# Kernel tuning notes

Hardware: AMD Instinct MI355X
Metric: run time of the kernel (lower is better)

Reference implementation:

```python
import jax, jax.numpy as jnp
import numpy as np

EPS = 1e-6
NUM_HEADS = 16


def _layernorm(x, g, b):
    m = jnp.mean(x, axis=-1, keepdims=True)
    v = jnp.mean(jnp.square(x - m), axis=-1, keepdims=True)
    return (x - m) * jax.lax.rsqrt(v + EPS) * g + b


def setup_inputs() -> dict:
    key = jax.random.key(0)
    ks = jax.random.split(key, 16)
    B, Lq, Lkv, D = 2, 2048, 4096, 2048
    Hd = D // NUM_HEADS
    s = 0.02
    return {
        "hidden_states": jax.random.normal(ks[0], (B, Lq, D), jnp.float32),
        "cross_attention_states": jax.random.normal(ks[1], (B, Lkv, D), jnp.float32),
        "q_w": jax.random.normal(ks[2], (D, D), jnp.float32) * s,
        "q_b": jnp.zeros((D,), jnp.float32),
        "k_w": jax.random.normal(ks[3], (D, D), jnp.float32) * s,
        "k_b": jnp.zeros((D,), jnp.float32),
        "v_w": jax.random.normal(ks[4], (D, D), jnp.float32) * s,
        "v_b": jnp.zeros((D,), jnp.float32),
        "o_w": jax.random.normal(ks[5], (D, D), jnp.float32) * s,
        "o_b": jnp.zeros((D,), jnp.float32),
        "qn_g": jnp.ones((Hd,), jnp.float32),
        "qn_b": jnp.zeros((Hd,), jnp.float32),
        "kn_g": jnp.ones((Hd,), jnp.float32),
        "kn_b": jnp.zeros((Hd,), jnp.float32),
    }


def reference(hidden_states, cross_attention_states,
              q_w, q_b, k_w, k_b, v_w, v_b, o_w, o_b,
              qn_g, qn_b, kn_g, kn_b):
    B, Lq, D = hidden_states.shape
    H = NUM_HEADS
    Hd = D // H
    scale = Hd ** -0.5

    # torch Linear: y = x @ W^T + b
    q = hidden_states @ q_w.T + q_b                        # [B,Lq,D]
    k = cross_attention_states @ k_w.T + k_b               # [B,Lkv,D]
    v = cross_attention_states @ v_w.T + v_b               # [B,Lkv,D]

    q = q.reshape(B, Lq, H, Hd).transpose(0, 2, 1, 3)      # [B,H,Lq,Hd]
    k = k.reshape(B, -1, H, Hd).transpose(0, 2, 1, 3)      # [B,H,Lkv,Hd]
    v = v.reshape(B, -1, H, Hd).transpose(0, 2, 1, 3)      # [B,H,Lkv,Hd]

    # per-head QK LayerNorm before scores
    q = _layernorm(q, qn_g, qn_b)
    k = _layernorm(k, kn_g, kn_b)

    attn_weights = jnp.einsum('bhqd,bhkd->bhqk', q, k) * scale
    attn_weights = jax.nn.softmax(attn_weights.astype(jnp.float32), axis=-1).astype(q.dtype)
    # dropout p=0.0 (inference) -> identity

    attn_output = jnp.einsum('bhqk,bhkd->bhqd', attn_weights, v)
    attn_output = attn_output.transpose(0, 2, 1, 3).reshape(B, Lq, D)
    attn_output = attn_output @ o_w.T + o_b
    return attn_output, attn_weights
```

## Files before the change

kernel.cpp:

```cpp
#include <hip/hip_runtime.h>
#include <cstdint>
#include <cstddef>

using u16 = unsigned short;
using f32x4 = __attribute__((ext_vector_type(4))) float;
using bf8   = __attribute__((ext_vector_type(8))) short;
using u32x4 = __attribute__((ext_vector_type(4))) unsigned;

#define DEVFN __device__ __forceinline__

constexpr int BB  = 2;
constexpr int LQ  = 2048;
constexpr int LKV = 4096;
constexpr int DD  = 2048;
constexpr int NH  = 16;
constexpr int HDm = 128;
constexpr float ATTN_SCALE = 0.08838834764831845f;
constexpr float LN_EPS = 1e-6f;
constexpr float LOG2E  = 1.4426950408889634f;
constexpr float SHIFT2 = 17.312340490667562f;

DEVFN u16 f2bf(float f) {
  unsigned u = __builtin_bit_cast(unsigned, f);
  u += 0x7fffu + ((u >> 16) & 1u);
  return (u16)(u >> 16);
}
DEVFN float bf2f(u16 h) { return __builtin_bit_cast(float, (unsigned)h << 16); }
DEVFN f32x4 mfma16(bf8 a, bf8 b, f32x4 c) {
  return __builtin_amdgcn_mfma_f32_16x16x32_bf16(a, b, c, 0, 0, 0);
}
DEVFN void gl16(const void* g, void* l) {
  __builtin_amdgcn_global_load_lds(
      (const __attribute__((address_space(1))) void*)g,
      (__attribute__((address_space(3))) void*)l, 16, 0, 0);
}
DEVFN void barrier_hard() {
  __builtin_amdgcn_s_barrier();
  __builtin_amdgcn_sched_barrier(0);
}

__global__ __launch_bounds__(256) void k_cvt(const float4* __restrict__ in,
                                             ushort4* __restrict__ out, int n4) {
  int i = blockIdx.x * 256 + threadIdx.x;
  if (i >= n4) return;
  float4 v = in[i];
  ushort4 o;
  o.x = f2bf(v.x); o.y = f2bf(v.y); o.z = f2bf(v.z); o.w = f2bf(v.w);
  out[i] = o;
}

template <int MODE>
__global__ __launch_bounds__(256) void k_gemm_nt(const u16* __restrict__ X,
                                                 const u16* __restrict__ Wt,
                                                 const float* __restrict__ bias,
                                                 const float* __restrict__ lng,
                                                 const float* __restrict__ lnb,
                                                 void* __restrict__ Y,
                                                 int M, int N, int K) {
  __shared__ __align__(16) u16 Sh[2][128 * 64];
  __shared__ float Sm[2][128], Sq[2][128];
  u16* As = Sh[0];
  u16* Bs = Sh[1];
  const int tid = threadIdx.x;
  const int w = tid >> 6, l = tid & 63;
  const int m0 = blockIdx.x * 128, n0 = blockIdx.y * 128;
  const int wr = w >> 1, wc = w & 1;
  const int lr = l & 15, lk = (l >> 4) * 8;
  const int rsw = (l & 7) << 3;
  const int srow = l >> 3;
  const int scb = (l & 7) * 16;
  f32x4 acc[4][4] = {};

  for (int k0 = 0; k0 < K; k0 += 64) {
#pragma unroll
    for (int i = 0; i < 4; ++i) {
      int rbase = w * 32 + i * 8;
      int row = rbase + srow;
      int cb = scb ^ ((row & 7) << 4);
      gl16((const char*)&X[(size_t)(m0 + row) * K + k0] + cb, &As[rbase * 64]);
      gl16((const char*)&Wt[(size_t)(n0 + row) * K + k0] + cb, &Bs[rbase * 64]);
    }
    __syncthreads();
    bf8 af[4][2], bfr[4][2];
#pragma unroll
    for (int mi = 0; mi < 4; ++mi)
#pragma unroll
      for (int kk = 0; kk < 2; ++kk)
        af[mi][kk] = *(const bf8*)&As[(wr * 64 + mi * 16 + lr) * 64 + ((kk * 32 + lk) ^ rsw)];
#pragma unroll
    for (int ni = 0; ni < 4; ++ni)
#pragma unroll
      for (int kk = 0; kk < 2; ++kk)
        bfr[ni][kk] = *(const bf8*)&Bs[(wc * 64 + ni * 16 + lr) * 64 + ((kk * 32 + lk) ^ rsw)];
#pragma unroll
    for (int kk = 0; kk < 2; ++kk)
#pragma unroll
      for (int mi = 0; mi < 4; ++mi)
#pragma unroll
        for (int ni = 0; ni < 4; ++ni)
          acc[mi][ni] = mfma16(af[mi][kk], bfr[ni][kk], acc[mi][ni]);
    __syncthreads();
  }
  const int lrg = (l >> 4) * 4;

  float bv[4];
#pragma unroll
  for (int ni = 0; ni < 4; ++ni) bv[ni] = bias[n0 + wc * 64 + ni * 16 + lr];
#pragma unroll
  for (int mi = 0; mi < 4; ++mi)
#pragma unroll
    for (int ni = 0; ni < 4; ++ni)
#pragma unroll
      for (int r = 0; r < 4; ++r) acc[mi][ni][r] += bv[ni];

  if constexpr (MODE == 2 || MODE == 3) {
#pragma unroll
    for (int mi = 0; mi < 4; ++mi) {
#pragma unroll
      for (int r = 0; r < 4; ++r) {
        float ps = 0.f, pq = 0.f;
#pragma unroll
        for (int ni = 0; ni < 4; ++ni) {
          float v = acc[mi][ni][r];
          ps += v; pq += v * v;
        }
#pragma unroll
        for (int m = 1; m < 16; m <<= 1) {
          ps += __shfl_xor(ps, m);
          pq += __shfl_xor(pq, m);
        }
        if (lr == 0) {
          int rl = wr * 64 + mi * 16 + lrg + r;
          Sm[wc][rl] = ps; Sq[wc][rl] = pq;
        }
      }
    }
    __syncthreads();
    float gv[4], bbv[4];
#pragma unroll
    for (int ni = 0; ni < 4; ++ni) {
      int c = wc * 64 + ni * 16 + lr;
      gv[ni] = lng[c]; bbv[ni] = lnb[c];
    }
#pragma unroll
    for (int mi = 0; mi < 4; ++mi)
#pragma unroll
      for (int r = 0; r < 4; ++r) {
        int rl = wr * 64 + mi * 16 + lrg + r;
        float mean = (Sm[0][rl] + Sm[1][rl]) * (1.f / 128.f);
        float var  = (Sq[0][rl] + Sq[1][rl]) * (1.f / 128.f) - mean * mean;
        float rs = rsqrtf(var + LN_EPS);
#pragma unroll
        for (int ni = 0; ni < 4; ++ni) {
          float o = (acc[mi][ni][r] - mean) * rs * gv[ni] + bbv[ni];
          if (MODE == 3) o *= ATTN_SCALE;
          acc[mi][ni][r] = o;
        }
      }
  }

  if constexpr (MODE == 4) {
    u16* T = &Sh[0][0];
#pragma unroll
    for (int mi = 0; mi < 4; ++mi)
#pragma unroll
      for (int ni = 0; ni < 4; ++ni)
#pragma unroll
        for (int r = 0; r < 4; ++r) {
          int mrow = wr * 64 + mi * 16 + lrg + r;
          int ncol = wc * 64 + ni * 16 + lr;
          T[mrow * 128 + (ncol ^ ((mrow & 7) << 3))] = f2bf(acc[mi][ni][r]);
        }
    __syncthreads();
    int hd = tid >> 1, half = tid & 1;
    int bq = m0 >> 12;
    int kvb = (m0 & (LKV - 1)) + half * 64;
    int hh = n0 >> 7;
    u16* vout = (u16*)Y + ((size_t)(bq * NH + hh) * HDm + hd) * LKV + kvb;
#pragma unroll
    for (int j8 = 0; j8 < 8; ++j8) {
      u16 tmp[8] __attribute__((aligned(16)));
#pragma unroll
      for (int j = 0; j < 8; ++j) {
        int kv = half * 64 + j8 * 8 + j;
        tmp[j] = T[kv * 128 + (hd ^ ((kv & 7) << 3))];
      }
      *(int4*)&vout[j8 * 8] = *(const int4*)tmp;
    }
    return;
  }

#pragma unroll
  for (int ni = 0; ni < 4; ++ni) {
    int n = n0 + wc * 64 + ni * 16 + lr;
#pragma unroll
    for (int mi = 0; mi < 4; ++mi) {
      int mb = m0 + wr * 64 + mi * 16 + lrg;
#pragma unroll
      for (int r = 0; r < 4; ++r) {
        float v = acc[mi][ni][r];
        if constexpr (MODE == 1)
          __builtin_nontemporal_store(v, &((float*)Y)[(size_t)(mb + r) * N + n]);
        else
          ((u16*)Y)[(size_t)(mb + r) * N + n] = f2bf(v);
      }
    }
  }
}

__global__ __launch_bounds__(512, 4) void k_attn(const u16* __restrict__ Qp,
                                                 const u16* __restrict__ Kp,
                                                 const u16* __restrict__ Vt,
                                                 float* __restrict__ Wout,
                                                 u16* __restrict__ AO) {
  const int g = blockIdx.x;
  const int work = (g & 7) * 64 + (g >> 3);
  const int bh = work >> 4;
  const int b = bh >> 4, h = bh & 15;
  const int q0 = (work & 15) * 128;
  const int tid = threadIdx.x, w = tid >> 6, l = tid & 63;
  const int lr = l & 15, lk = (l >> 4) * 8;
  const int gq = l >> 4;
  const int rsw = (l & 7) << 3;
  __shared__ __align__(16) u16 Ks[2][64 * 128];
  __shared__ __align__(16) u16 Vs[2][128 * 64];

  bf8 qf[4];
  {
    const u16* qb = &Qp[((size_t)b * LQ + q0 + w * 16 + lr) * DD + h * HDm];
#pragma unroll
    for (int kc = 0; kc < 4; ++kc) qf[kc] = *(const bf8*)(qb + kc * 32 + lk);
  }
  const u16* Kb = Kp + (size_t)b * LKV * DD + h * HDm;
  const u16* Vb = Vt + (size_t)bh * HDm * LKV;

  auto stageK128 = [&](u16* buf, int kv0) {
#pragma unroll
    for (int i = 0; i < 4; ++i) {
      int rbase = i * 32 + w * 4;
      int row = rbase + (l >> 4);
      int cb = ((l & 15) * 16) ^ ((row & 7) << 4);
      gl16((const char*)(Kb + (size_t)(kv0 + row) * DD) + cb, &buf[rbase * 128]);
    }
  };
  auto stageK = [&](int buf, int kv0) {
#pragma unroll
    for (int i = 0; i < 2; ++i) {
      int rbase = i * 32 + w * 4;
      int row = rbase + (l >> 4);
      int cb = ((l & 15) * 16) ^ ((row & 7) << 4);
      gl16((const char*)(Kb + (size_t)(kv0 + row) * DD) + cb, &Ks[buf][rbase * 128]);
    }
  };
  auto stageV = [&](int buf, int kv0) {
#pragma unroll
    for (int i = 0; i < 2; ++i) {
      int rbase = i * 64 + w * 8;
      int row = rbase + (l >> 3);
      int cb = ((l & 7) * 16) ^ ((row & 7) << 4);
      gl16((const char*)(Vb + (size_t)row * LKV + kv0) + cb, &Vs[buf][rbase * 64]);
    }
  };

  u16* bufA0 = &Ks[0][0];
  u16* bufA1 = &Vs[0][0];
  float lsum = 0.f;
  stageK128(bufA0, 0);
  asm volatile("s_waitcnt vmcnt(0)" ::: "memory");
  barrier_hard();
  for (int t = 0; t < 32; ++t) {
    const u16* kb = (t & 1) ? bufA1 : bufA0;
    if (t < 31) stageK128((t & 1) ? bufA0 : bufA1, (t + 1) * 128);
    f32x4 s8[8];
    __builtin_amdgcn_s_setprio(1);
#pragma unroll
    for (int ni = 0; ni < 8; ++ni) {
      s8[ni] = f32x4{0.f, 0.f, 0.f, 0.f};
#pragma unroll
      for (int kc = 0; kc < 4; ++kc) {
        bf8 kf = *(const bf8*)&kb[(ni * 16 + lr) * 128 + ((kc * 32 + lk) ^ rsw)];
        s8[ni] = mfma16(kf, qf[kc], s8[ni]);
      }
    }
    __builtin_amdgcn_s_setprio(0);
#pragma unroll
    for (int ni = 0; ni < 8; ++ni)
#pragma unroll
      for (int r = 0; r < 4; ++r)
        lsum += exp2f(fmaf(s8[ni][r], LOG2E, -SHIFT2));
    asm volatile("s_waitcnt vmcnt(0)" ::: "memory");
    barrier_hard();
  }
  lsum += __shfl_xor(lsum, 16);
  lsum += __shfl_xor(lsum, 32);
  const float cr = -(SHIFT2 + __log2f(lsum));

  f32x4 oacc[8] = {};
  float* wq = Wout + ((size_t)bh * LQ + q0 + w * 16 + lr) * LKV;
  const int srcA = lr + ((gq & 1) << 5);
  const int srcB = srcA + 16;
  const bool hi = (gq >> 1) != 0;

  stageK(0, 0); stageV(0, 0);
  asm volatile("s_waitcnt vmcnt(0)" ::: "memory");
  barrier_hard();
  for (int t = 0; t < 64; ++t) {
    const int cur = t & 1;
    const int kv0 = t * 64;
    if (t < 63) { stageK(cur ^ 1, kv0 + 64); stageV(cur ^ 1, kv0 + 64); }
    f32x4 s[4];
    __builtin_amdgcn_s_setprio(1);
#pragma unroll
    for (int ni = 0; ni < 4; ++ni) {
      s[ni] = f32x4{0.f, 0.f, 0.f, 0.f};
#pragma unroll
      for (int kc = 0; kc < 4; ++kc) {
        bf8 kf = *(const bf8*)&Ks[cur][(ni * 16 + lr) * 128 + ((kc * 32 + lk) ^ rsw)];
        s[ni] = mfma16(kf, qf[kc], s[ni]);
      }
    }
    __builtin_amdgcn_s_setprio(0);
    unsigned pk2[4][2];
#pragma unroll
    for (int ni = 0; ni < 4; ++ni) {
      float p0 = exp2f(fmaf(s[ni][0], LOG2E, cr));
      float p1 = exp2f(fmaf(s[ni][1], LOG2E, cr));
      float p2 = exp2f(fmaf(s[ni][2], LOG2E, cr));
      float p3 = exp2f(fmaf(s[ni][3], LOG2E, cr));
      f32x4 pv4 = {p0, p1, p2, p3};
      __builtin_nontemporal_store(pv4, (f32x4*)(wq + kv0 + ni * 16 + 4 * gq));
      pk2[ni][0] = (unsigned)f2bf(p0) | ((unsigned)f2bf(p1) << 16);
      pk2[ni][1] = (unsigned)f2bf(p2) | ((unsigned)f2bf(p3) << 16);
    }
#pragma unroll
    for (int kk = 0; kk < 2; ++kk) {
      unsigned xa0 = __shfl(pk2[2 * kk][0], srcA), xa1 = __shfl(pk2[2 * kk][1], srcA);
      unsigned ya0 = __shfl(pk2[2 * kk + 1][0], srcA), ya1 = __shfl(pk2[2 * kk + 1][1], srcA);
      unsigned xb0 = __shfl(pk2[2 * kk][0], srcB), xb1 = __shfl(pk2[2 * kk][1], srcB);
      unsigned yb0 = __shfl(pk2[2 * kk + 1][0], srcB), yb1 = __shfl(pk2[2 * kk + 1][1], srcB);
      u32x4 pf32 = { hi ? ya0 : xa0, hi ? ya1 : xa1, hi ? yb0 : xb0, hi ? yb1 : xb1 };
      bf8 pf = __builtin_bit_cast(bf8, pf32);
      __builtin_amdgcn_s_setprio(1);
#pragma unroll
      for (int c = 0; c < 8; ++c) {
        bf8 vf = *(const bf8*)&Vs[cur][(c * 16 + lr) * 64 + ((kk * 32 + lk) ^ rsw)];
        oacc[c] = mfma16(pf, vf, oacc[c]);
      }
      __builtin_amdgcn_s_setprio(0);
    }
    asm volatile("s_waitcnt vmcnt(4)" ::: "memory");
    barrier_hard();
  }

#pragma unroll
  for (int c = 0; c < 8; ++c)
#pragma unroll
    for (int r = 0; r < 4; ++r)
      AO[((size_t)b * LQ + q0 + w * 16 + 4 * gq + r) * DD + h * HDm + c * 16 + lr] =
          f2bf(oacc[c][r]);
}

extern "C" void kernel_launch(void* const* d_in, const int* in_sizes, int n_in,
                              void* d_out, int out_size, void* d_ws, size_t ws_size,
                              hipStream_t stream) {
  const float* hs   = (const float*)d_in[0];
  const float* cas  = (const float*)d_in[1];
  const float* q_w  = (const float*)d_in[2];
  const float* q_b  = (const float*)d_in[3];
  const float* k_w  = (const float*)d_in[4];
  const float* k_b  = (const float*)d_in[5];
  const float* v_w  = (const float*)d_in[6];
  const float* v_b  = (const float*)d_in[7];
  const float* o_w  = (const float*)d_in[8];
  const float* o_b  = (const float*)d_in[9];
  const float* qn_g = (const float*)d_in[10];
  const float* qn_b = (const float*)d_in[11];
  const float* kn_g = (const float*)d_in[12];
  const float* kn_b = (const float*)d_in[13];

  float* out_attn = (float*)d_out;
  float* out_w    = out_attn + (size_t)BB * LQ * DD;

  constexpr size_t SZ_Q  = (size_t)BB * LQ * DD * 2;
  constexpr size_t SZ_KV = (size_t)BB * LKV * DD * 2;
  constexpr size_t SZ_W  = (size_t)DD * DD * 2;
  char* p = (char*)d_ws;
  u16* hsb  = (u16*)p;              p += SZ_Q;
  u16* casb = (u16*)p;              p += SZ_KV;
  u16* qwb  = (u16*)p;              p += SZ_W;
  u16* kwb  = (u16*)p;              p += SZ_W;
  u16* vwb  = (u16*)p;              p += SZ_W;
  u16* owb  = (u16*)p;              p += SZ_W;
  u16* Qp   = (u16*)p;              p += SZ_Q;
  u16* Kp   = (u16*)p;              p += SZ_KV;
  u16* Vtp  = (u16*)p;              p += SZ_KV;
  u16* AO   = (u16*)p;              p += SZ_Q;

  auto cvt = [&](const float* src, u16* dst, size_t n) {
    int n4 = (int)(n / 4);
    k_cvt<<<dim3((n4 + 255) / 256), dim3(256), 0, stream>>>(
        (const float4*)src, (ushort4*)dst, n4);
  };
  cvt(hs,  hsb,  (size_t)BB * LQ * DD);
  cvt(cas, casb, (size_t)BB * LKV * DD);
  cvt(q_w, qwb, (size_t)DD * DD);
  cvt(k_w, kwb, (size_t)DD * DD);
  cvt(v_w, vwb, (size_t)DD * DD);
  cvt(o_w, owb, (size_t)DD * DD);

  k_gemm_nt<3><<<dim3(BB * LQ / 128, DD / 128), dim3(256), 0, stream>>>(
      hsb, qwb, q_b, qn_g, qn_b, Qp, BB * LQ, DD, DD);
  k_gemm_nt<2><<<dim3(BB * LKV / 128, DD / 128), dim3(256), 0, stream>>>(
      casb, kwb, k_b, kn_g, kn_b, Kp, BB * LKV, DD, DD);
  k_gemm_nt<4><<<dim3(BB * LKV / 128, DD / 128), dim3(256), 0, stream>>>(
      casb, vwb, v_b, nullptr, nullptr, Vtp, BB * LKV, DD, DD);

  k_attn<<<dim3(LQ / 128 * BB * NH), dim3(512), 0, stream>>>(Qp, Kp, Vtp, out_w, AO);

  k_gemm_nt<1><<<dim3(BB * LQ / 128, DD / 128), dim3(256), 0, stream>>>(
      AO, owb, o_b, nullptr, nullptr, out_attn, BB * LQ, DD, DD);
}
```

Baseline: 753.5 us.

## Give each attention wave two 16-row Q tiles to reuse K/V fragments

The attention kernel drops from 8 to 4 waves per block. Each wave now handles 32 query rows as two 16-row sub-tiles, so every K and V fragment read from LDS feeds two MFMAs instead of one. Staging loops are rebalanced to load the same tiles with fewer threads, and the wait count is adjusted to match. This halves LDS read traffic per MFMA but doubles accumulator registers, and dropping the occupancy hint may lower occupancy and latency hiding.

After: 760.1 us. Within noise of the previous version (+0.9%).

```diff
diff --git a/kernel.cpp b/kernel.cpp
--- a/kernel.cpp
+++ b/kernel.cpp
@@ -208,11 +208,11 @@
   }
 }
 
-__global__ __launch_bounds__(512, 4) void k_attn(const u16* __restrict__ Qp,
-                                                 const u16* __restrict__ Kp,
-                                                 const u16* __restrict__ Vt,
-                                                 float* __restrict__ Wout,
-                                                 u16* __restrict__ AO) {
+__global__ __launch_bounds__(256) void k_attn(const u16* __restrict__ Qp,
+                                              const u16* __restrict__ Kp,
+                                              const u16* __restrict__ Vt,
+                                              float* __restrict__ Wout,
+                                              u16* __restrict__ AO) {
   const int g = blockIdx.x;
   const int work = (g & 7) * 64 + (g >> 3);
   const int bh = work >> 4;
@@ -225,78 +225,85 @@
   __shared__ __align__(16) u16 Ks[2][64 * 128];
   __shared__ __align__(16) u16 Vs[2][128 * 64];
 
-  bf8 qf[4];
-  {
-    const u16* qb = &Qp[((size_t)b * LQ + q0 + w * 16 + lr) * DD + h * HDm];
-#pragma unroll
-    for (int kc = 0; kc < 4; ++kc) qf[kc] = *(const bf8*)(qb + kc * 32 + lk);
+  bf8 qf[2][4];
+#pragma unroll
+  for (int qc = 0; qc < 2; ++qc) {
+    const u16* qb = &Qp[((size_t)b * LQ + q0 + w * 32 + qc * 16 + lr) * DD + h * HDm];
+#pragma unroll
+    for (int kc = 0; kc < 4; ++kc) qf[qc][kc] = *(const bf8*)(qb + kc * 32 + lk);
   }
   const u16* Kb = Kp + (size_t)b * LKV * DD + h * HDm;
   const u16* Vb = Vt + (size_t)bh * HDm * LKV;
 
+  auto stageK = [&](int buf, int kv0) {
+#pragma unroll
+    for (int i = 0; i < 4; ++i) {
+      int rbase = w * 16 + i * 4;
+      int row = rbase + (l >> 4);
+      int cb = ((l & 15) * 16) ^ ((row & 7) << 4);
+      gl16((const char*)(Kb + (size_t)(kv0 + row) * DD) + cb, &Ks[buf][rbase * 128]);
+    }
+  };
+  auto stageV = [&](int buf, int kv0) {
+#pragma unroll
+    for (int i = 0; i < 4; ++i) {
+      int rbase = w * 32 + i * 8;
+      int row = rbase + (l >> 3);
+      int cb = ((l & 7) * 16) ^ ((row & 7) << 4);
+      gl16((const char*)(Vb + (size_t)row * LKV + kv0) + cb, &Vs[buf][rbase * 64]);
+    }
+  };
   auto stageK128 = [&](u16* buf, int kv0) {
 #pragma unroll
-    for (int i = 0; i < 4; ++i) {
-      int rbase = i * 32 + w * 4;
+    for (int i = 0; i < 8; ++i) {
+      int rbase = w * 32 + i * 4;
       int row = rbase + (l >> 4);
       int cb = ((l & 15) * 16) ^ ((row & 7) << 4);
       gl16((const char*)(Kb + (size_t)(kv0 + row) * DD) + cb, &buf[rbase * 128]);
     }
   };
-  auto stageK = [&](int buf, int kv0) {
-#pragma unroll
-    for (int i = 0; i < 2; ++i) {
-      int rbase = i * 32 + w * 4;
-      int row = rbase + (l >> 4);
-      int cb = ((l & 15) * 16) ^ ((row & 7) << 4);
-      gl16((const char*)(Kb + (size_t)(kv0 + row) * DD) + cb, &Ks[buf][rbase * 128]);
-    }
-  };
-  auto stageV = [&](int buf, int kv0) {
-#pragma unroll
-    for (int i = 0; i < 2; ++i) {
-      int rbase = i * 64 + w * 8;
-      int row = rbase + (l >> 3);
-      int cb = ((l & 7) * 16) ^ ((row & 7) << 4);
-      gl16((const char*)(Vb + (size_t)row * LKV + kv0) + cb, &Vs[buf][rbase * 64]);
-    }
-  };
 
   u16* bufA0 = &Ks[0][0];
   u16* bufA1 = &Vs[0][0];
-  float lsum = 0.f;
+  float lsum[2] = {0.f, 0.f};
   stageK128(bufA0, 0);
   asm volatile("s_waitcnt vmcnt(0)" ::: "memory");
   barrier_hard();
   for (int t = 0; t < 32; ++t) {
     const u16* kb = (t & 1) ? bufA1 : bufA0;
     if (t < 31) stageK128((t & 1) ? bufA0 : bufA1, (t + 1) * 128);
-    f32x4 s8[8];
-    __builtin_amdgcn_s_setprio(1);
 #pragma unroll
     for (int ni = 0; ni < 8; ++ni) {
-      s8[ni] = f32x4{0.f, 0.f, 0.f, 0.f};
+      f32x4 s0 = {0.f, 0.f, 0.f, 0.f}, s1 = {0.f, 0.f, 0.f, 0.f};
+      __builtin_amdgcn_s_setprio(1);
 #pragma unroll
       for (int kc = 0; kc < 4; ++kc) {
         bf8 kf = *(const bf8*)&kb[(ni * 16 + lr) * 128 + ((kc * 32 + lk) ^ rsw)];
-        s8[ni] = mfma16(kf, qf[kc], s8[ni]);
-      }
-    }
-    __builtin_amdgcn_s_setprio(0);
-#pragma unroll
-    for (int ni = 0; ni < 8; ++ni)
-#pragma unroll
-      for (int r = 0; r < 4; ++r)
-        lsum += exp2f(fmaf(s8[ni][r], LOG2E, -SHIFT2));
+        s0 = mfma16(kf, qf[0][kc], s0);
+        s1 = mfma16(kf, qf[1][kc], s1);
+      }
+      __builtin_amdgcn_s_setprio(0);
+#pragma unroll
+      for (int r = 0; r < 4; ++r) {
+        lsum[0] += exp2f(fmaf(s0[r], LOG2E, -SHIFT2));
+        lsum[1] += exp2f(fmaf(s1[r], LOG2E, -SHIFT2));
+      }
+    }
     asm volatile("s_waitcnt vmcnt(0)" ::: "memory");
     barrier_hard();
   }
-  lsum += __shfl_xor(lsum, 16);
-  lsum += __shfl_xor(lsum, 32);
-  const float cr = -(SHIFT2 + __log2f(lsum));
-
-  f32x4 oacc[8] = {};
-  float* wq = Wout + ((size_t)bh * LQ + q0 + w * 16 + lr) * LKV;
+  float cr[2];
+#pragma unroll
+  for (int qc = 0; qc < 2; ++qc) {
+    float v = lsum[qc];
+    v += __shfl_xor(v, 16);
+    v += __shfl_xor(v, 32);
+    cr[qc] = -(SHIFT2 + __log2f(v));
+  }
+
+  f32x4 oacc[2][8] = {};
+  float* wq0 = Wout + ((size_t)bh * LQ + q0 + w * 32 + lr) * LKV;
+  float* wq1 = wq0 + (size_t)16 * LKV;
   const int srcA = lr + ((gq & 1) << 5);
   const int srcB = srcA + 16;
   const bool hi = (gq >> 1) != 0;
@@ -308,56 +315,69 @@
     const int cur = t & 1;
     const int kv0 = t * 64;
     if (t < 63) { stageK(cur ^ 1, kv0 + 64); stageV(cur ^ 1, kv0 + 64); }
-    f32x4 s[4];
+    f32x4 s[2][4];
     __builtin_amdgcn_s_setprio(1);
 #pragma unroll
     for (int ni = 0; ni < 4; ++ni) {
-      s[ni] = f32x4{0.f, 0.f, 0.f, 0.f};
+      s[0][ni] = f32x4{0.f, 0.f, 0.f, 0.f};
+      s[1][ni] = f32x4{0.f, 0.f, 0.f, 0.f};
 #pragma unroll
       for (int kc = 0; kc < 4; ++kc) {
         bf8 kf = *(const bf8*)&Ks[cur][(ni * 16 + lr) * 128 + ((kc * 32 + lk) ^ rsw)];
-        s[ni] = mfma16(kf, qf[kc], s[ni]);
+        s[0][ni] = mfma16(kf, qf[0][kc], s[0][ni]);
+        s[1][ni] = mfma16(kf, qf[1][kc], s[1][ni]);
       }
     }
     __builtin_amdgcn_s_setprio(0);
-    unsigned pk2[4][2];
-#pragma unroll
-    for (int ni = 0; ni < 4; ++ni) {
-      float p0 = exp2f(fmaf(s[ni][0], LOG2E, cr));
-      float p1 = exp2f(fmaf(s[ni][1], LOG2E, cr));
-      float p2 = exp2f(fmaf(s[ni][2], LOG2E, cr));
-      float p3 = exp2f(fmaf(s[ni][3], LOG2E, cr));
-      f32x4 pv4 = {p0, p1, p2, p3};
-      __builtin_nontemporal_store(pv4, (f32x4*)(wq + kv0 + ni * 16 + 4 * gq));
-      pk2[ni][0] = (unsigned)f2bf(p0) | ((unsigned)f2bf(p1) << 16);
-      pk2[ni][1] = (unsigned)f2bf(p2) | ((unsigned)f2bf(p3) << 16);
+    unsigned pk2[2][4][2];
+#pragma unroll
+    for (int qc = 0; qc < 2; ++qc) {
+      float* wq = qc ? wq1 : wq0;
+#pragma unroll
+      for (int ni = 0; ni < 4; ++ni) {
+        float p0 = exp2f(fmaf(s[qc][ni][0], LOG2E, cr[qc]));
+        float p1 = exp2f(fmaf(s[qc][ni][1], LOG2E, cr[qc]));
+        float p2 = exp2f(fmaf(s[qc][ni][2], LOG2E, cr[qc]));
+        float p3 = exp2f(fmaf(s[qc][ni][3], LOG2E, cr[qc]));
+        f32x4 pv4 = {p0, p1, p2, p3};
+        __builtin_nontemporal_store(pv4, (f32x4*)(wq + kv0 + ni * 16 + 4 * gq));
+        pk2[qc][ni][0] = (unsigned)f2bf(p0) | ((unsigned)f2bf(p1) << 16);
+        pk2[qc][ni][1] = (unsigned)f2bf(p2) | ((unsigned)f2bf(p3) << 16);
+      }
     }
 #pragma unroll
     for (int kk = 0; kk < 2; ++kk) {
-      unsigned xa0 = __shfl(pk2[2 * kk][0], srcA), xa1 = __shfl(pk2[2 * kk][1], srcA);
-      unsigned ya0 = __shfl(pk2[2 * kk + 1][0], srcA), ya1 = __shfl(pk2[2 * kk + 1][1], srcA);
-      unsigned xb0 = __shfl(pk2[2 * kk][0], srcB), xb1 = __shfl(pk2[2 * kk][1], srcB);
-      unsigned yb0 = __shfl(pk2[2 * kk + 1][0], srcB), yb1 = __shfl(pk2[2 * kk + 1][1], srcB);
-      u32x4 pf32 = { hi ? ya0 : xa0, hi ? ya1 : xa1, hi ? yb0 : xb0, hi ? yb1 : xb1 };
-      bf8 pf = __builtin_bit_cast(bf8, pf32);
+      bf8 pfq[2];
+#pragma unroll
+      for (int qc = 0; qc < 2; ++qc) {
+        unsigned xa0 = __shfl(pk2[qc][2 * kk][0], srcA), xa1 = __shfl(pk2[qc][2 * kk][1], srcA);
+        unsigned ya0 = __shfl(pk2[qc][2 * kk + 1][0], srcA), ya1 = __shfl(pk2[qc][2 * kk + 1][1], srcA);
+        unsigned xb0 = __shfl(pk2[qc][2 * kk][0], srcB), xb1 = __shfl(pk2[qc][2 * kk][1], srcB);
+        unsigned yb0 = __shfl(pk2[qc][2 * kk + 1][0], srcB), yb1 = __shfl(pk2[qc][2 * kk + 1][1], srcB);
+        u32x4 pf32 = { hi ? ya0 : xa0, hi ? ya1 : xa1, hi ? yb0 : xb0, hi ? yb1 : xb1 };
+        pfq[qc] = __builtin_bit_cast(bf8, pf32);
+      }
       __builtin_amdgcn_s_setprio(1);
 #pragma unroll
       for (int c = 0; c < 8; ++c) {
         bf8 vf = *(const bf8*)&Vs[cur][(c * 16 + lr) * 64 + ((kk * 32 + lk) ^ rsw)];
-        oacc[c] = mfma16(pf, vf, oacc[c]);
+        oacc[0][c] = mfma16(pfq[0], vf, oacc[0][c]);
+        oacc[1][c] = mfma16(pfq[1], vf, oacc[1][c]);
       }
       __builtin_amdgcn_s_setprio(0);
     }
-    asm volatile("s_waitcnt vmcnt(4)" ::: "memory");
+    asm volatile("s_waitcnt vmcnt(8)" ::: "memory");
     barrier_hard();
   }
 
 #pragma unroll
-  for (int c = 0; c < 8; ++c)
-#pragma unroll
-    for (int r = 0; r < 4; ++r)
-      AO[((size_t)b * LQ + q0 + w * 16 + 4 * gq + r) * DD + h * HDm + c * 16 + lr] =
-          f2bf(oacc[c][r]);
+  for (int qc = 0; qc < 2; ++qc)
+#pragma unroll
+    for (int c = 0; c < 8; ++c)
+#pragma unroll
+      for (int r = 0; r < 4; ++r)
+        AO[((size_t)b * LQ + q0 + w * 32 + qc * 16 + 4 * gq + r) * DD + h * HDm + c * 16 + lr] =
+            f2bf(oacc[qc][c][r]);
 }
 
 extern "C" void kernel_launch(void* const* d_in, const int* in_sizes, int n_in,
@@ -415,7 +435,7 @@
   k_gemm_nt<4><<<dim3(BB * LKV / 128, DD / 128), dim3(256), 0, stream>>>(
       casb, vwb, v_b, nullptr, nullptr, Vtp, BB * LKV, DD, DD);
 
-  k_attn<<<dim3(LQ / 128 * BB * NH), dim3(512), 0, stream>>>(Qp, Kp, Vtp, out_w, AO);
+  k_attn<<<dim3(LQ / 128 * BB * NH), dim3(256), 0, stream>>>(Qp, Kp, Vtp, out_w, AO);
 
   k_gemm_nt<1><<<dim3(BB * LQ / 128, DD / 128), dim3(256), 0, stream>>>(
       AO, owb, o_b, nullptr, nullptr, out_attn, BB * LQ, DD, DD);
```

## Split softmax row-sum pass into separate kernel with 256-row Q tiles; fuse conversions

Applied to the files above, without the earlier changes.

The first pass that computes softmax normalisers moves out of the attention kernel into its own kernel. That kernel processes 256 query rows per block and keeps two Q fragments per wave, so each staged K tile is reused twice. It writes per-row log constants to a workspace buffer, which the attention kernel then reads. The six fp32-to-bf16 conversion launches are merged into one segmented launch. This halves K reloads in the sum pass and removes launch overhead, at the cost of an extra kernel launch, a small global buffer, and a larger LDS footprint per block.

Result: slower. 796.2 us (+5.7%).

```diff
diff --git a/kernel.cpp b/kernel.cpp
--- a/kernel.cpp
+++ b/kernel.cpp
@@ -39,14 +39,22 @@
   __builtin_amdgcn_sched_barrier(0);
 }
 
-__global__ __launch_bounds__(256) void k_cvt(const float4* __restrict__ in,
-                                             ushort4* __restrict__ out, int n4) {
-  int i = blockIdx.x * 256 + threadIdx.x;
-  if (i >= n4) return;
-  float4 v = in[i];
+struct C6 {
+  const float4* s[6];
+  ushort4* d[6];
+  unsigned off[7];
+};
+__global__ __launch_bounds__(256) void k_cvt6(C6 a) {
+  unsigned gi = blockIdx.x * 256 + threadIdx.x;
+  if (gi >= a.off[6]) return;
+  int seg = 0;
+#pragma unroll
+  for (int i = 1; i < 6; ++i) seg += (gi >= a.off[i]);
+  unsigned j = gi - a.off[seg];
+  float4 v = a.s[seg][j];
   ushort4 o;
   o.x = f2bf(v.x); o.y = f2bf(v.y); o.z = f2bf(v.z); o.w = f2bf(v.w);
-  out[i] = o;
+  a.d[seg][j] = o;
 }
 
 template <int MODE>
@@ -208,9 +216,79 @@
   }
 }
 
+__global__ __launch_bounds__(512, 4) void k_sums(const u16* __restrict__ Qp,
+                                                 const u16* __restrict__ Kp,
+                                                 float* __restrict__ crg) {
+  const int g = blockIdx.x;
+  const int work = (g & 7) * 32 + (g >> 3);
+  const int bh = work >> 3;
+  const int b = bh >> 4, h = bh & 15;
+  const int q0 = (work & 7) * 256;
+  const int tid = threadIdx.x, w = tid >> 6, l = tid & 63;
+  const int lr = l & 15, lk = (l >> 4) * 8;
+  const int rsw = (l & 7) << 3;
+  __shared__ __align__(16) u16 Kt[2][128 * 128];
+
+  bf8 qf[2][4];
+#pragma unroll
+  for (int qc = 0; qc < 2; ++qc) {
+    const u16* qb = &Qp[((size_t)b * LQ + q0 + w * 32 + qc * 16 + lr) * DD + h * HDm];
+#pragma unroll
+    for (int kc = 0; kc < 4; ++kc) qf[qc][kc] = *(const bf8*)(qb + kc * 32 + lk);
+  }
+  const u16* Kb = Kp + (size_t)b * LKV * DD + h * HDm;
+
+  auto stage = [&](int buf, int kv0) {
+#pragma unroll
+    for (int i = 0; i < 4; ++i) {
+      int rbase = w * 16 + i * 4;
+      int row = rbase + (l >> 4);
+      int cb = ((l & 15) * 16) ^ ((row & 7) << 4);
+      gl16((const char*)(Kb + (size_t)(kv0 + row) * DD) + cb, &Kt[buf][rbase * 128]);
+    }
+  };
+
+  float lsum[2] = {0.f, 0.f};
+  stage(0, 0);
+  asm volatile("s_waitcnt vmcnt(0)" ::: "memory");
+  barrier_hard();
+  for (int t = 0; t < 32; ++t) {
+    const int cur = t & 1;
+    if (t < 31) stage(cur ^ 1, (t + 1) * 128);
+#pragma unroll
+    for (int ni = 0; ni < 8; ++ni) {
+      f32x4 s0 = {0.f, 0.f, 0.f, 0.f}, s1 = {0.f, 0.f, 0.f, 0.f};
+      __builtin_amdgcn_s_setprio(1);
+#pragma unroll
+      for (int kc = 0; kc < 4; ++kc) {
+        bf8 kf = *(const bf8*)&Kt[cur][(ni * 16 + lr) * 128 + ((kc * 32 + lk) ^ rsw)];
+        s0 = mfma16(kf, qf[0][kc], s0);
+        s1 = mfma16(kf, qf[1][kc], s1);
+      }
+      __builtin_amdgcn_s_setprio(0);
+#pragma unroll
+      for (int r = 0; r < 4; ++r) {
+        lsum[0] += exp2f(fmaf(s0[r], LOG2E, -SHIFT2));
+        lsum[1] += exp2f(fmaf(s1[r], LOG2E, -SHIFT2));
+      }
+    }
+    asm volatile("s_waitcnt vmcnt(0)" ::: "memory");
+    barrier_hard();
+  }
+#pragma unroll
+  for (int qc = 0; qc < 2; ++qc) {
+    float v = lsum[qc];
+    v += __shfl_xor(v, 16);
+    v += __shfl_xor(v, 32);
+    if (l < 16)
+      crg[(size_t)bh * LQ + q0 + w * 32 + qc * 16 + l] = -(SHIFT2 + __log2f(v));
+  }
+}
+
 __global__ __launch_bounds__(512, 4) void k_attn(const u16* __restrict__ Qp,
                                                  const u16* __restrict__ Kp,
                                                  const u16* __restrict__ Vt,
+                                                 const float* __restrict__ crg,
                                                  float* __restrict__ Wout,
                                                  u16* __restrict__ AO) {
   const int g = blockIdx.x;
@@ -231,18 +309,10 @@
 #pragma unroll
     for (int kc = 0; kc < 4; ++kc) qf[kc] = *(const bf8*)(qb + kc * 32 + lk);
   }
+  const float crv = crg[(size_t)bh * LQ + q0 + w * 16 + lr];
   const u16* Kb = Kp + (size_t)b * LKV * DD + h * HDm;
   const u16* Vb = Vt + (size_t)bh * HDm * LKV;
 
-  auto stageK128 = [&](u16* buf, int kv0) {
-#pragma unroll
-    for (int i = 0; i < 4; ++i) {
-      int rbase = i * 32 + w * 4;
-      int row = rbase + (l >> 4);
-      int cb = ((l & 15) * 16) ^ ((row & 7) << 4);
-      gl16((const char*)(Kb + (size_t)(kv0 + row) * DD) + cb, &buf[rbase * 128]);
-    }
-  };
   auto stageK = [&](int buf, int kv0) {
 #pragma unroll
     for (int i = 0; i < 2; ++i) {
@@ -261,39 +331,6 @@
       gl16((const char*)(Vb + (size_t)row * LKV + kv0) + cb, &Vs[buf][rbase * 64]);
     }
   };
-
-  u16* bufA0 = &Ks[0][0];
-  u16* bufA1 = &Vs[0][0];
-  float lsum = 0.f;
-  stageK128(bufA0, 0);
-  asm volatile("s_waitcnt vmcnt(0)" ::: "memory");
-  barrier_hard();
-  for (int t = 0; t < 32; ++t) {
-    const u16* kb = (t & 1) ? bufA1 : bufA0;
-    if (t < 31) stageK128((t & 1) ? bufA0 : bufA1, (t + 1) * 128);
-    f32x4 s8[8];
-    __builtin_amdgcn_s_setprio(1);
-#pragma unroll
-    for (int ni = 0; ni < 8; ++ni) {
-      s8[ni] = f32x4{0.f, 0.f, 0.f, 0.f};
-#pragma unroll
-      for (int kc = 0; kc < 4; ++kc) {
-        bf8 kf = *(const bf8*)&kb[(ni * 16 + lr) * 128 + ((kc * 32 + lk) ^ rsw)];
-        s8[ni] = mfma16(kf, qf[kc], s8[ni]);
-      }
-    }
-    __builtin_amdgcn_s_setprio(0);
-#pragma unroll
-    for (int ni = 0; ni < 8; ++ni)
-#pragma unroll
-      for (int r = 0; r < 4; ++r)
-        lsum += exp2f(fmaf(s8[ni][r], LOG2E, -SHIFT2));
-    asm volatile("s_waitcnt vmcnt(0)" ::: "memory");
-    barrier_hard();
-  }
-  lsum += __shfl_xor(lsum, 16);
-  lsum += __shfl_xor(lsum, 32);
-  const float cr = -(SHIFT2 + __log2f(lsum));
 
   f32x4 oacc[8] = {};
   float* wq = Wout + ((size_t)bh * LQ + q0 + w * 16 + lr) * LKV;
@@ -323,10 +360,10 @@
     unsigned pk2[4][2];
 #pragma unroll
     for (int ni = 0; ni < 4; ++ni) {
-      float p0 = exp2f(fmaf(s[ni][0], LOG2E, cr));
-      float p1 = exp2f(fmaf(s[ni][1], LOG2E, cr));
-      float p2 = exp2f(fmaf(s[ni][2], LOG2E, cr));
-      float p3 = exp2f(fmaf(s[ni][3], LOG2E, cr));
+      float p0 = exp2f(fmaf(s[ni][0], LOG2E, crv));
+      float p1 = exp2f(fmaf(s[ni][1], LOG2E, crv));
+      float p2 = exp2f(fmaf(s[ni][2], LOG2E, crv));
+      float p3 = exp2f(fmaf(s[ni][3], LOG2E, crv));
       f32x4 pv4 = {p0, p1, p2, p3};
       __builtin_nontemporal_store(pv4, (f32x4*)(wq + kv0 + ni * 16 + 4 * gq));
       pk2[ni][0] = (unsigned)f2bf(p0) | ((unsigned)f2bf(p1) << 16);
@@ -395,18 +432,26 @@
   u16* Kp   = (u16*)p;              p += SZ_KV;
   u16* Vtp  = (u16*)p;              p += SZ_KV;
   u16* AO   = (u16*)p;              p += SZ_Q;
-
-  auto cvt = [&](const float* src, u16* dst, size_t n) {
-    int n4 = (int)(n / 4);
-    k_cvt<<<dim3((n4 + 255) / 256), dim3(256), 0, stream>>>(
-        (const float4*)src, (ushort4*)dst, n4);
-  };
-  cvt(hs,  hsb,  (size_t)BB * LQ * DD);
-  cvt(cas, casb, (size_t)BB * LKV * DD);
-  cvt(q_w, qwb, (size_t)DD * DD);
-  cvt(k_w, kwb, (size_t)DD * DD);
-  cvt(v_w, vwb, (size_t)DD * DD);
-  cvt(o_w, owb, (size_t)DD * DD);
+  float* crg = (float*)p;           p += (size_t)BB * NH * LQ * 4;
+
+  constexpr unsigned HS4 = BB * LQ * DD / 4;
+  constexpr unsigned CAS4 = BB * LKV * DD / 4;
+  constexpr unsigned W4 = DD * DD / 4;
+  C6 a;
+  a.s[0] = (const float4*)hs;  a.d[0] = (ushort4*)hsb;
+  a.s[1] = (const float4*)cas; a.d[1] = (ushort4*)casb;
+  a.s[2] = (const float4*)q_w; a.d[2] = (ushort4*)qwb;
+  a.s[3] = (const float4*)k_w; a.d[3] = (ushort4*)kwb;
+  a.s[4] = (const float4*)v_w; a.d[4] = (ushort4*)vwb;
+  a.s[5] = (const float4*)o_w; a.d[5] = (ushort4*)owb;
+  a.off[0] = 0;
+  a.off[1] = HS4;
+  a.off[2] = HS4 + CAS4;
+  a.off[3] = HS4 + CAS4 + W4;
+  a.off[4] = HS4 + CAS4 + 2 * W4;
+  a.off[5] = HS4 + CAS4 + 3 * W4;
+  a.off[6] = HS4 + CAS4 + 4 * W4;
+  k_cvt6<<<dim3((a.off[6] + 255) / 256), dim3(256), 0, stream>>>(a);
 
   k_gemm_nt<3><<<dim3(BB * LQ / 128, DD / 128), dim3(256), 0, stream>>>(
       hsb, qwb, q_b, qn_g, qn_b, Qp, BB * LQ, DD, DD);
@@ -415,7 +460,10 @@
   k_gemm_nt<4><<<dim3(BB * LKV / 128, DD / 128), dim3(256), 0, stream>>>(
       casb, vwb, v_b, nullptr, nullptr, Vtp, BB * LKV, DD, DD);
 
-  k_attn<<<dim3(LQ / 128 * BB * NH), dim3(512), 0, stream>>>(Qp, Kp, Vtp, out_w, AO);
+  k_sums<<<dim3(LQ / 256 * BB * NH), dim3(512), 0, stream>>>(Qp, Kp, crg);
+
+  k_attn<<<dim3(LQ / 128 * BB * NH), dim3(512), 0, stream>>>(
+      Qp, Kp, Vtp, crg, out_w, AO);
 
   k_gemm_nt<1><<<dim3(BB * LQ / 128, DD / 128), dim3(256), 0, stream>>>(
       AO, owb, o_b, nullptr, nullptr, out_attn, BB * LQ, DD, DD);
```
